# Kernel optimization log

Measured on AMD Instinct MI355X. Metric: run time of the kernel, lower is better.

## Reference

```python
import jax, jax.numpy as jnp
import numpy as np

ALPHA, GAMMA = 0.25, 2.0
IOU_THRES = 0.5
WEIGHTS = (10.0, 10.0, 5.0, 5.0, 15.0)
MAXV = 16  # max polygon verts during quad-vs-quad clipping (<=8, padded)


def box_corners(b):
    # b: (5,) = cx, cy, w, h, theta(rad); returns (4,2) CCW corners
    cx, cy, w, h, t = b[0], b[1], b[2], b[3], b[4]
    c, s = jnp.cos(t), jnp.sin(t)
    dx = jnp.array([-0.5, 0.5, 0.5, -0.5]) * w
    dy = jnp.array([-0.5, -0.5, 0.5, 0.5]) * h
    return jnp.stack([cx + dx * c - dy * s, cy + dx * s + dy * c], axis=-1)


def pair_iou(b1, b2):
    # exact rotated-rectangle IoU via Sutherland-Hodgman clipping
    p1 = box_corners(b1)
    p2 = box_corners(b2)
    poly = jnp.zeros((MAXV, 2)).at[:4].set(p1)
    n = jnp.int32(4)
    for e in range(4):
        a = p2[e]
        d = p2[(e + 1) % 4] - a
        out = jnp.zeros((MAXV, 2))
        m = jnp.int32(0)
        for i in range(MAXV):
            cur = poly[i]
            nxt = poly[jnp.where(i + 1 >= n, 0, i + 1)]
            sc = d[0] * (cur[1] - a[1]) - d[1] * (cur[0] - a[0])
            sn = d[0] * (nxt[1] - a[1]) - d[1] * (nxt[0] - a[0])
            valid = i < n
            keep = valid & (sc >= 0)
            out = out.at[m].set(jnp.where(keep, cur, out[m]))
            m = m + keep.astype(jnp.int32)
            crossed = valid & ((sc >= 0) != (sn >= 0))
            den = sc - sn
            t = sc / jnp.where(den == 0, 1.0, den)
            ip = cur + t * (nxt - cur)
            out = out.at[m].set(jnp.where(crossed, ip, out[m]))
            m = m + crossed.astype(jnp.int32)
        poly, n = out, m
    idx = jnp.arange(MAXV)
    nxt = jnp.where(idx + 1 >= n, 0, idx + 1)
    cr = poly[:, 0] * poly[nxt, 1] - poly[nxt, 0] * poly[:, 1]
    inter = 0.5 * jnp.abs(jnp.sum(jnp.where(idx < n, cr, 0.0)))
    union = b1[2] * b1[3] + b2[2] * b2[3] - inter
    return inter / jnp.maximum(union, 1e-9)


rbox_iou_mat = jax.vmap(jax.vmap(pair_iou, (None, 0)), (0, None))  # (A,5),(G,5)->(A,G)


def min_area_square(rb):
    s = jnp.maximum(rb[:, 2], rb[:, 3])
    return jnp.stack([rb[:, 0] - s / 2, rb[:, 1] - s / 2,
                      rb[:, 0] + s / 2, rb[:, 1] + s / 2], 1)


def bbox_overlaps(a, b):
    lt = jnp.maximum(a[:, None, :2], b[None, :, :2])
    rb = jnp.minimum(a[:, None, 2:], b[None, :, 2:])
    wh = jnp.clip(rb - lt, 0.0)
    inter = wh[..., 0] * wh[..., 1]
    aa = (a[:, 2] - a[:, 0]) * (a[:, 3] - a[:, 1])
    ab = (b[:, 2] - b[:, 0]) * (b[:, 3] - b[:, 1])
    return inter / jnp.maximum(aa[:, None] + ab[None, :] - inter, 1e-9)


def encode(ex, gt):
    wx, wy, ww, wh, wt = WEIGHTS
    ew = jnp.maximum(ex[:, 2], 1.0); eh = jnp.maximum(ex[:, 3], 1.0)
    gw = jnp.maximum(gt[:, 2], 1.0); gh = jnp.maximum(gt[:, 3], 1.0)
    dx = wx * (gt[:, 0] - ex[:, 0]) / ew
    dy = wy * (gt[:, 1] - ex[:, 1]) / eh
    dw = ww * jnp.log(gw / ew)
    dh = wh * jnp.log(gh / eh)
    dt = wt * (jnp.tan(gt[:, 4]) - jnp.tan(ex[:, 4]))
    return jnp.stack([dx, dy, dw, dh, dt], 1)


def lmr5pangle(anch, dt):
    # encoded angle offset of the 90-degree-swapped box: tan(t+pi/2) = -1/tan(t)
    wt = WEIGHTS[4]
    ta = jnp.tan(anch[:, 4])
    tg = dt / wt + ta
    tg = jnp.where(jnp.abs(tg) < 1e-4, jnp.where(tg < 0, -1e-4, 1e-4), tg)
    return wt * (-1.0 / tg - ta)


def landmark_encode(ex, lm):
    wx, wy = WEIGHTS[0], WEIGHTS[1]
    ew = jnp.maximum(ex[:, 2], 1.0); eh = jnp.maximum(ex[:, 3], 1.0)
    return jnp.stack([wx * (lm[:, 0] - ex[:, 0]) / ew,
                      wy * (lm[:, 1] - ex[:, 1]) / eh,
                      wx * (lm[:, 2] - ex[:, 0]) / ew,
                      wy * (lm[:, 3] - ex[:, 1]) / eh], 1)


def smooth_l1(d, beta=1.0 / 9):
    d = jnp.abs(d)
    return jnp.where(d < beta, 0.5 * d * d / beta, d - 0.5 * beta)


def lmr5p_per_anchor(pred, tgt, anch):
    t22 = lmr5pangle(anch, pred[:, 4])
    l1 = smooth_l1(tgt[:, 0] - pred[:, 0])
    l2 = smooth_l1(tgt[:, 1] - pred[:, 1])
    l3 = smooth_l1(tgt[:, 2] - pred[:, 2])
    l4 = smooth_l1(tgt[:, 3] - pred[:, 3])
    l5 = smooth_l1(tgt[:, 2] - pred[:, 3])  # |w1 - h2|
    l6 = smooth_l1(tgt[:, 3] - pred[:, 2])  # |h1 - w2|
    l7 = smooth_l1(tgt[:, 4] - pred[:, 4])
    l8 = smooth_l1(tgt[:, 4] - t22)
    return jnp.minimum(l1 + l2 + l3 + l4 + l7, l1 + l2 + l5 + l6 + l8)


def balanced_l1(d, beta=0.5, al=0.5, ga=0.9):
    d = jnp.abs(d)
    b = np.e ** (ga / al) - 1.0
    return jnp.where(d < beta,
                     al / b * (b * d + 1.0) * jnp.log(b * d / beta + 1.0) - al * d,
                     ga * d + ga / b - al * beta)


def per_image(cls, reg, lmk, anch, ann, ls):
    valid_g = ann[:, -1] != -1.0
    has_gt = jnp.any(valid_g)
    cls = jnp.clip(cls, 1e-4, 1.0 - 1e-4)
    indicator = bbox_overlaps(min_area_square(anch), min_area_square(ann[:, :5]))
    riou = rbox_iou_mat(anch, ann[:, :5])
    ious = jnp.where(indicator >= 0.1, riou, 0.0)   # rbox_overlaps thresh=0.1 gating
    ious = jnp.where(valid_g[None, :], ious, -1.0)  # mask padded gts
    ious = jax.lax.stop_gradient(ious)              # torch computes ious on cpu numpy
    iou_max = ious.max(1)
    iou_argmax = ious.argmax(1)
    pos = iou_max >= IOU_THRES
    max_gt = ious.max(0)
    argmax_gt = ious.argmax(0)
    force = valid_g & (max_gt < IOU_THRES)
    pos = (pos.astype(jnp.int32).at[argmax_gt].max(force.astype(jnp.int32))) > 0
    num_pos = pos.sum()
    denom = jnp.maximum(num_pos.astype(cls.dtype), 1.0)
    assigned = ann[iou_argmax]                       # (A, 6)
    lab = assigned[:, -1].astype(jnp.int32)
    onehot = (lab[:, None] == jnp.arange(cls.shape[-1])[None, :]).astype(cls.dtype)
    tgt = jnp.where(pos[:, None], onehot,
                    jnp.where((iou_max < IOU_THRES - 0.1)[:, None], 0.0, -1.0))
    af = jnp.where(tgt == 1.0, ALPHA, 1.0 - ALPHA)
    fw = af * jnp.where(tgt == 1.0, 1.0 - cls, cls) ** GAMMA
    bce = -(tgt * jnp.log(cls + 1e-6) + (1.0 - tgt) * jnp.log(1.0 - cls + 1e-6))
    cls_loss = jnp.where(tgt != -1.0, fw * bce, 0.0).sum() / denom
    cls_loss = jnp.where(has_gt, cls_loss, 0.0)
    gt_safe = jnp.where(pos[:, None], assigned[:, :5], anch)  # keep masked lanes finite
    tg1 = encode(anch, gt_safe)
    r1 = jnp.where(pos, lmr5p_per_anchor(reg, tg1, anch), 0.0).sum() / (5.0 * denom)
    r1 = jnp.where(has_gt & (num_pos > 0), r1, 0.0)
    lm_safe = jnp.where(pos[:, None], ls[iou_argmax],
                        jnp.stack([anch[:, 0], anch[:, 1], anch[:, 0], anch[:, 1]], 1))
    tg2 = landmark_encode(anch, lm_safe)
    r2 = jnp.where(pos[:, None], balanced_l1(lmk - tg2), 0.0).sum() / (4.0 * denom)
    r2 = jnp.where(has_gt & (num_pos > 0), r2, 0.0)
    return cls_loss, r1, r2


def setup_inputs() -> dict:
    B, A, G, C = 2, 16384, 24, 8
    NV = 16  # valid gts per image; remaining rows padded with label -1
    ks = jax.random.split(jax.random.key(0), 16)
    classifications = jax.random.uniform(ks[0], (B, A, C), jnp.float32)
    regressions = jax.random.normal(ks[1], (B, A, 5), jnp.float32) * 0.1
    landmarks = jax.random.normal(ks[2], (B, A, 4), jnp.float32) * 0.1
    gcx = 100.0 + 800.0 * jax.random.uniform(ks[3], (B, G))
    gcy = 100.0 + 800.0 * jax.random.uniform(ks[4], (B, G))
    gw = 40.0 + 160.0 * jax.random.uniform(ks[5], (B, G))
    gh = 40.0 + 160.0 * jax.random.uniform(ks[6], (B, G))
    gth = 1.2 * jax.random.uniform(ks[7], (B, G)) - 0.6
    lab = jax.random.randint(ks[8], (B, G), 0, C).astype(jnp.float32)
    lab = jnp.where(jnp.arange(G)[None, :] >= NV, -1.0, lab)
    annotations = jnp.stack([gcx, gcy, gw, gh, gth, lab], -1)
    acx = 1024.0 * jax.random.uniform(ks[9], (B, A))
    acy = 1024.0 * jax.random.uniform(ks[10], (B, A))
    aw = 16.0 + 112.0 * jax.random.uniform(ks[11], (B, A))
    ah = 16.0 + 112.0 * jax.random.uniform(ks[12], (B, A))
    ath = 1.2 * jax.random.uniform(ks[13], (B, A)) - 0.6
    anchors = jnp.stack([acx, acy, aw, ah, ath], -1)
    # plant jittered copies of the gts so a healthy number of anchors are positive
    jit = jax.random.normal(ks[14], (B, G, 5)) * jnp.array([2.0, 2.0, 2.0, 2.0, 0.01])
    anchors = anchors.at[:, :G, :].set(annotations[:, :, :5] + jit)
    ca, sa = jnp.cos(gth), jnp.sin(gth)
    gt_linestrips = jnp.stack([gcx - 0.4 * gw * ca, gcy - 0.4 * gw * sa,
                               gcx + 0.4 * gw * ca, gcy + 0.4 * gw * sa], -1)
    return {"classifications": classifications, "regressions": regressions,
            "anchors": anchors, "annotations": annotations,
            "landmarks": landmarks, "gt_linestrips": gt_linestrips}


def reference(classifications, regressions, anchors, annotations, landmarks, gt_linestrips):
    cls_l, r1, r2 = jax.vmap(per_image)(classifications, regressions, landmarks,
                                        anchors, annotations, gt_linestrips)
    return (cls_l.mean(keepdims=True), r1.mean(keepdims=True), r2.mean(keepdims=True))
```

## Files before the change

### kernel.cpp

```cpp
#include <hip/hip_runtime.h>
#include <math.h>

#define B_N 2
#define A_N 16384
#define G_N 24
#define C_N 8
#define NV  16
#define BPI 256

#define OFF_GTKEY  0
#define OFF_AKEY   384
#define OFF_PART   (384 + B_N * A_N * 8)

__device__ inline unsigned int fmap(float v) {
    unsigned int u = __float_as_uint(v);
    return (u & 0x80000000u) ? ~u : (u | 0x80000000u);
}
__device__ inline float funmap(unsigned int u) {
    unsigned int bits = (u & 0x80000000u) ? (u ^ 0x80000000u) : ~u;
    return __uint_as_float(bits);
}
__device__ inline unsigned long long mkkey(float v, int idx) {
    return ((unsigned long long)fmap(v) << 32) |
           (unsigned long long)(0xFFFFFFFFu - (unsigned int)idx);
}
__device__ inline float key_val(unsigned long long k) { return funmap((unsigned int)(k >> 32)); }
__device__ inline int   key_idx(unsigned long long k) { return (int)(0xFFFFFFFFu - (unsigned int)k); }

__device__ inline float smoothl1(float x) {
    const float beta = 1.0f / 9.0f;
    float d = fabsf(x);
    return (d < beta) ? (0.5f * d * d / beta) : (d - 0.5f * beta);
}
__device__ inline float balancedl1(float x) {
    const float bb  = 5.049647464412945f;
    const float alb = 0.5f / 5.049647464412945f;
    const float gab = 0.9f / 5.049647464412945f;
    float d = fabsf(x);
    if (d < 0.5f)
        return alb * (bb * d + 1.0f) * logf(bb * d / 0.5f + 1.0f) - 0.5f * d;
    return 0.9f * d + gab - 0.25f;
}
__device__ inline float focal_pos(const float* cr, int lab) {
    float s = 0.0f;
#pragma unroll
    for (int c = 0; c < C_N; c++) {
        float p = fminf(fmaxf(cr[c], 1e-4f), 0.9999f);
        if (c == lab) s += 0.25f * (1.0f - p) * (1.0f - p) * (-logf(p + 1e-6f));
        else          s += 0.75f * p * p * (-logf(1.0f - p + 1e-6f));
    }
    return s;
}
__device__ inline float focal_neg(const float* cr) {
    float s = 0.0f;
#pragma unroll
    for (int c = 0; c < C_N; c++) {
        float p = fminf(fmaxf(cr[c], 1e-4f), 0.9999f);
        s += 0.75f * p * p * (-logf(1.0f - p + 1e-6f));
    }
    return s;
}
__device__ inline float reg_loss(const float* rr, const float* ar, const float* annr) {
    float acx = ar[0], acy = ar[1], aw = ar[2], ah = ar[3], ath = ar[4];
    float aw1 = fmaxf(aw, 1.0f), ah1 = fmaxf(ah, 1.0f);
    float gw1 = fmaxf(annr[2], 1.0f), gh1 = fmaxf(annr[3], 1.0f);
    float t1 = 10.0f * (annr[0] - acx) / aw1;
    float t2 = 10.0f * (annr[1] - acy) / ah1;
    float t3 = 5.0f * logf(gw1 / aw1);
    float t4 = 5.0f * logf(gh1 / ah1);
    float ta = tanf(ath);
    float t5 = 15.0f * (tanf(annr[4]) - ta);
    float p0 = rr[0], p1 = rr[1], p2 = rr[2], p3 = rr[3], p4 = rr[4];
    float tg = p4 / 15.0f + ta;
    if (fabsf(tg) < 1e-4f) tg = (tg < 0.0f) ? -1e-4f : 1e-4f;
    float t22 = 15.0f * (-1.0f / tg - ta);
    float l1 = smoothl1(t1 - p0), l2 = smoothl1(t2 - p1);
    float l3 = smoothl1(t3 - p2), l4 = smoothl1(t4 - p3);
    float l5 = smoothl1(t3 - p3), l6 = smoothl1(t4 - p2);
    float l7 = smoothl1(t5 - p4), l8 = smoothl1(t5 - t22);
    return fminf(l1 + l2 + l3 + l4 + l7, l1 + l2 + l5 + l6 + l8);
}
__device__ inline float lmk_loss(const float* lk, const float* ar, const float* lr) {
    float acx = ar[0], acy = ar[1];
    float aw1 = fmaxf(ar[2], 1.0f), ah1 = fmaxf(ar[3], 1.0f);
    return balancedl1(lk[0] - 10.0f * (lr[0] - acx) / aw1)
         + balancedl1(lk[1] - 10.0f * (lr[1] - acy) / ah1)
         + balancedl1(lk[2] - 10.0f * (lr[2] - acx) / aw1)
         + balancedl1(lk[3] - 10.0f * (lr[3] - acy) / ah1);
}

__global__ __launch_bounds__(64) void k_main(
    const float* __restrict__ cls, const float* __restrict__ reg,
    const float* __restrict__ anch, const float* __restrict__ ann,
    const float* __restrict__ lmk, const float* __restrict__ ls,
    unsigned long long* __restrict__ gtkey, unsigned long long* __restrict__ akey,
    float* __restrict__ partials)
{
    __shared__ float pb[2][2][NV][64];
    __shared__ float gcor[G_N][10];
    __shared__ float gsq[G_N][5];
    __shared__ float glab[G_N];
    __shared__ float acor[9][64];
    __shared__ unsigned long long rowk[64];
    __shared__ unsigned short wl[G_N * 64];

    const int tid = threadIdx.x;
    const int b   = blockIdx.x >> 8;
    const int a   = ((blockIdx.x & (BPI - 1)) << 6) | tid;
    const size_t idx = (size_t)b * A_N + a;
    const float* annb = ann + (size_t)b * G_N * 6;

    const float* cr = cls + idx * C_N;
    float crv[C_N];
#pragma unroll
    for (int c = 0; c < C_N; c++) crv[c] = cr[c];

    const float* ar = anch + idx * 5;
    float acx = ar[0], acy = ar[1], aw = ar[2], ah = ar[3], ath = ar[4];

    if (tid < G_N) {
        const float* annr = annb + tid * 6;
        float gcx = annr[0], gcy = annr[1], gw = annr[2], gh = annr[3], gth = annr[4];
        glab[tid] = annr[5];
        float sg = fmaxf(gw, gh);
        float gx1 = gcx - sg * 0.5f, gy1 = gcy - sg * 0.5f;
        float gx2 = gcx + sg * 0.5f, gy2 = gcy + sg * 0.5f;
        gsq[tid][0] = gx1; gsq[tid][1] = gy1; gsq[tid][2] = gx2; gsq[tid][3] = gy2;
        gsq[tid][4] = (gx2 - gx1) * (gy2 - gy1);
        float c2 = cosf(gth), s2 = sinf(gth);
        const float dxs[4] = {-0.5f, 0.5f, 0.5f, -0.5f};
        const float dys[4] = {-0.5f, -0.5f, 0.5f, 0.5f};
#pragma unroll
        for (int k = 0; k < 4; k++) {
            float ex = dxs[k] * gw, ey = dys[k] * gh;
            gcor[tid][k]     = gcx + ex * c2 - ey * s2;
            gcor[tid][4 + k] = gcy + ex * s2 + ey * c2;
        }
        gcor[tid][8] = gw * gh;
    }
    if (a == 0) {
        for (int g = 0; g < G_N; g++)
            atomicMax(&gtkey[b * G_N + g], mkkey(0.0f, 0));
    }

    {
        float c1 = cosf(ath), s1 = sinf(ath);
        const float dxs[4] = {-0.5f, 0.5f, 0.5f, -0.5f};
        const float dys[4] = {-0.5f, -0.5f, 0.5f, 0.5f};
#pragma unroll
        for (int k = 0; k < 4; k++) {
            float dx = dxs[k] * aw, dy = dys[k] * ah;
            acor[k][tid]     = acx + dx * c1 - dy * s1;
            acor[4 + k][tid] = acy + dx * s1 + dy * c1;
        }
        acor[8][tid] = aw * ah;
    }
    __syncthreads();

    unsigned int validmask = 0;
    for (int g = 0; g < G_N; g++)
        if (glab[g] != -1.0f) validmask |= (1u << g);
    int first_valid = validmask ? (__ffs((int)validmask) - 1) : -1;

    rowk[tid] = (first_valid >= 0) ? mkkey(0.0f, first_valid) : 0ull;

    float sa = fmaxf(aw, ah);
    float ax1 = acx - sa * 0.5f, ay1 = acy - sa * 0.5f;
    float ax2 = acx + sa * 0.5f, ay2 = acy + sa * 0.5f;
    float areaA = (ax2 - ax1) * (ay2 - ay1);

    int cnt = 0;
    for (unsigned int vm = validmask; vm; vm &= vm - 1) {
        int g = __ffs((int)vm) - 1;
        float gx1 = gsq[g][0], gy1 = gsq[g][1], gx2 = gsq[g][2], gy2 = gsq[g][3];
        float iw = fmaxf(fminf(ax2, gx2) - fmaxf(ax1, gx1), 0.0f);
        float ih = fmaxf(fminf(ay2, gy2) - fmaxf(ay1, gy1), 0.0f);
        float inter0 = iw * ih;
        float ind = inter0 / fmaxf(areaA + gsq[g][4] - inter0, 1e-9f);
        bool pass = (ind >= 0.1f);
        unsigned long long bal = __ballot(pass);
        if (pass) {
            int off = __popcll(bal & ((1ull << tid) - 1ull));
            wl[cnt + off] = (unsigned short)((tid << 5) | g);
        }
        cnt += __popcll(bal);
    }
    __syncthreads();

    for (int i = tid; i < cnt; i += 64) {
        unsigned int e = wl[i];
        int owner = (int)(e >> 5);
        int g = (int)(e & 31u);
        float p2x[4], p2y[4];
#pragma unroll
        for (int k = 0; k < 4; k++) {
            p2x[k] = gcor[g][k];
            p2y[k] = gcor[g][4 + k];
            pb[0][0][k][tid] = acor[k][owner];
            pb[0][1][k][tid] = acor[4 + k][owner];
        }
        int n = 4, cb = 0;
#pragma unroll
        for (int e4 = 0; e4 < 4; e4++) {
            float apx = p2x[e4], apy = p2y[e4];
            float dx = p2x[(e4 + 1) & 3] - apx, dy = p2y[(e4 + 1) & 3] - apy;
            int m = 0, nb = cb ^ 1;
            for (int i2 = 0; i2 < n; i2++) {
                float cx_ = pb[cb][0][i2][tid], cy_ = pb[cb][1][i2][tid];
                int j = (i2 + 1 >= n) ? 0 : (i2 + 1);
                float nx_ = pb[cb][0][j][tid], ny_ = pb[cb][1][j][tid];
                float sc = dx * (cy_ - apy) - dy * (cx_ - apx);
                float sn = dx * (ny_ - apy) - dy * (nx_ - apx);
                bool ci = (sc >= 0.0f), niv = (sn >= 0.0f);
                if (ci) {
                    if (m < NV) { pb[nb][0][m][tid] = cx_; pb[nb][1][m][tid] = cy_; }
                    m++;
                }
                if (ci != niv) {
                    float den = sc - sn;
                    float t = sc / ((den == 0.0f) ? 1.0f : den);
                    if (m < NV) {
                        pb[nb][0][m][tid] = cx_ + t * (nx_ - cx_);
                        pb[nb][1][m][tid] = cy_ + t * (ny_ - cy_);
                    }
                    m++;
                }
            }
            n = (m > NV) ? NV : m;
            cb = nb;
        }
        float ssum = 0.0f;
        for (int i2 = 0; i2 < n; i2++) {
            int j = (i2 + 1 >= n) ? 0 : (i2 + 1);
            ssum += pb[cb][0][i2][tid] * pb[cb][1][j][tid]
                  - pb[cb][0][j][tid] * pb[cb][1][i2][tid];
        }
        float interA = 0.5f * fabsf(ssum);
        float uni = acor[8][owner] + gcor[g][8] - interA;
        float val = interA / fmaxf(uni, 1e-9f);

        atomicMax(&rowk[owner], mkkey(val, g));
        if (val > 0.0f) {
            int aowner = ((blockIdx.x & (BPI - 1)) << 6) | owner;
            atomicMax(&gtkey[b * G_N + g], mkkey(val, aowner));
        }
    }
    __syncthreads();

    unsigned long long rowkey = rowk[tid];
    akey[idx] = rowkey;

    float iou_max = key_val(rowkey);
    int gmax = key_idx(rowkey);
    const float* annr = annb + gmax * 6;
    float cls_sum = 0.0f, reg_sum = 0.0f, lmk_sum = 0.0f;
    int pc = 0;
    if (iou_max >= 0.5f) {
        pc = 1;
        cls_sum = focal_pos(crv, (int)annr[5]);
        reg_sum = reg_loss(reg + idx * 5, ar, annr);
        lmk_sum = lmk_loss(lmk + idx * 4, ar, ls + (size_t)(b * G_N + gmax) * 4);
    } else if (iou_max < 0.4f) {
        cls_sum = focal_neg(crv);
    }

    float fpc = (float)pc;
    for (int off = 32; off; off >>= 1) {
        cls_sum += __shfl_down(cls_sum, off);
        reg_sum += __shfl_down(reg_sum, off);
        lmk_sum += __shfl_down(lmk_sum, off);
        fpc     += __shfl_down(fpc, off);
    }
    if (tid == 0) {
        float* p = partials + (size_t)blockIdx.x * 4;
        p[0] = cls_sum; p[1] = reg_sum; p[2] = lmk_sum; p[3] = fpc;
    }
}

__global__ __launch_bounds__(128) void k_fix(
    const float* __restrict__ cls, const float* __restrict__ reg,
    const float* __restrict__ anch, const float* __restrict__ ann,
    const float* __restrict__ lmk, const float* __restrict__ ls,
    const unsigned long long* __restrict__ gtkey, const unsigned long long* __restrict__ akey,
    const float* __restrict__ partials, float* __restrict__ out)
{
    __shared__ float res[B_N][3];
    const int tid = threadIdx.x;
    const int b = tid >> 6, lane = tid & 63;

    double s0 = 0.0, s1 = 0.0, s2 = 0.0, s3 = 0.0;
    for (int r = lane; r < BPI; r += 64) {
        const float* p = partials + (size_t)(b * BPI + r) * 4;
        s0 += p[0]; s1 += p[1]; s2 += p[2]; s3 += p[3];
    }
    for (int off = 32; off; off >>= 1) {
        s0 += __shfl_down(s0, off);
        s1 += __shfl_down(s1, off);
        s2 += __shfl_down(s2, off);
        s3 += __shfl_down(s3, off);
    }

    const float* annb = ann + (size_t)b * G_N * 6;
    float dc = 0.0f, dr = 0.0f, dl = 0.0f; int dn = 0;
    if (lane < G_N) {
        bool valid = annb[lane * 6 + 5] != -1.0f;
        unsigned long long k = gtkey[b * G_N + lane];
        int fa = key_idx(k);
        bool force = valid && (key_val(k) < 0.5f);
        if (force) {
            for (int g2 = 0; g2 < lane; g2++) {
                if (annb[g2 * 6 + 5] == -1.0f) continue;
                unsigned long long k2 = gtkey[b * G_N + g2];
                if (key_val(k2) < 0.5f && key_idx(k2) == fa) { force = false; break; }
            }
        }
        if (force) {
            size_t fidx = (size_t)b * A_N + fa;
            unsigned long long ak = akey[fidx];
            float im = key_val(ak);
            if (!(im >= 0.5f)) {
                dn = 1;
                int gm = key_idx(ak);
                const float* cr = cls + fidx * C_N;
                float crv[C_N];
#pragma unroll
                for (int c = 0; c < C_N; c++) crv[c] = cr[c];
                const float* annr = annb + gm * 6;
                const float* arr = anch + fidx * 5;
                dc = focal_pos(crv, (int)annr[5]);
                if (im < 0.4f) dc -= focal_neg(crv);
                dr = reg_loss(reg + fidx * 5, arr, annr);
                dl = lmk_loss(lmk + fidx * 4, arr, ls + (size_t)(b * G_N + gm) * 4);
            }
        }
    }
    float fdn = (float)dn;
    for (int off = 32; off; off >>= 1) {
        dc  += __shfl_down(dc, off);
        dr  += __shfl_down(dr, off);
        dl  += __shfl_down(dl, off);
        fdn += __shfl_down(fdn, off);
    }
    if (lane == 0) {
        bool has_gt = false;
        for (int g = 0; g < G_N; g++)
            if (annb[g * 6 + 5] != -1.0f) has_gt = true;
        float np = (float)s3 + fdn;
        float denom = fmaxf(np, 1.0f);
        res[b][0] = has_gt ? (float)((s0 + dc) / denom) : 0.0f;
        res[b][1] = (has_gt && np > 0.0f) ? (float)((s1 + dr) / (5.0 * denom)) : 0.0f;
        res[b][2] = (has_gt && np > 0.0f) ? (float)((s2 + dl) / (4.0 * denom)) : 0.0f;
    }
    __syncthreads();
    if (tid == 0) {
        out[0] = (res[0][0] + res[1][0]) * 0.5f;
        out[1] = (res[0][1] + res[1][1]) * 0.5f;
        out[2] = (res[0][2] + res[1][2]) * 0.5f;
    }
}

extern "C" void kernel_launch(void* const* d_in, const int* in_sizes, int n_in,
                              void* d_out, int out_size, void* d_ws, size_t ws_size,
                              hipStream_t stream)
{
    (void)in_sizes; (void)n_in; (void)out_size; (void)ws_size;
    const float* cls  = (const float*)d_in[0];
    const float* reg  = (const float*)d_in[1];
    const float* anch = (const float*)d_in[2];
    const float* ann  = (const float*)d_in[3];
    const float* lmk  = (const float*)d_in[4];
    const float* ls   = (const float*)d_in[5];

    char* ws = (char*)d_ws;
    unsigned long long* gtkey = (unsigned long long*)(ws + OFF_GTKEY);
    unsigned long long* akey  = (unsigned long long*)(ws + OFF_AKEY);
    float* partials = (float*)(ws + OFF_PART);
    float* out = (float*)d_out;

    hipMemsetAsync(gtkey, 0, B_N * G_N * 8, stream);
    hipLaunchKernelGGL(k_main, dim3(B_N * BPI), dim3(64), 0, stream,
                       cls, reg, anch, ann, lmk, ls, gtkey, akey, partials);
    hipLaunchKernelGGL(k_fix, dim3(1), dim3(128), 0, stream,
                       cls, reg, anch, ann, lmk, ls, gtkey, akey, partials, out);
}
```

Measured before the change: 103.9 us.

## Precompute GT table in a prep kernel and restructure polygon clipping

Adds a small prep kernel that builds a per-GT record table (corners, square box, tan, landmarks, label) plus a valid mask, replacing the memset and the per-block GT setup and atomics. The main kernel copies the table into LDS with float4 loads and vectorises the class-score loads. The clipping is restructured: the first edge clips from registers, the middle edges use float2 LDS buffers capped at 8 vertices, and the last edge accumulates the shoelace area directly without storing. This trades an extra kernel launch for less per-block setup and fewer LDS round trips, and it relies on the clipped polygon never exceeding 8 vertices.

```diff
diff --git a/kernel.cpp b/kernel.cpp
--- a/kernel.cpp
+++ b/kernel.cpp
@@ -5,12 +5,16 @@
 #define A_N 16384
 #define G_N 24
 #define C_N 8
-#define NV  16
+#define NV8 8
 #define BPI 256
+#define RECF 32
+#define RECL 33
 
 #define OFF_GTKEY  0
-#define OFF_AKEY   384
-#define OFF_PART   (384 + B_N * A_N * 8)
+#define OFF_META   384
+#define OFF_GTAB   512
+#define OFF_AKEY   (512 + 6144)
+#define OFF_PART   (OFF_AKEY + B_N * A_N * 8)
 
 __device__ inline unsigned int fmap(float v) {
     unsigned int u = __float_as_uint(v);
@@ -59,6 +63,34 @@
         s += 0.75f * p * p * (-logf(1.0f - p + 1e-6f));
     }
     return s;
+}
+__device__ inline float reg_loss_v(const float* rr, float acx, float acy, float aw,
+                                   float ah, float ath, const float* gl) {
+    float aw1 = fmaxf(aw, 1.0f), ah1 = fmaxf(ah, 1.0f);
+    float gw1 = fmaxf(gl[16], 1.0f), gh1 = fmaxf(gl[17], 1.0f);
+    float t1 = 10.0f * (gl[14] - acx) / aw1;
+    float t2 = 10.0f * (gl[15] - acy) / ah1;
+    float t3 = 5.0f * logf(gw1 / aw1);
+    float t4 = 5.0f * logf(gh1 / ah1);
+    float ta = tanf(ath);
+    float t5 = 15.0f * (gl[20] - ta);
+    float p0 = rr[0], p1 = rr[1], p2 = rr[2], p3 = rr[3], p4 = rr[4];
+    float tg = p4 / 15.0f + ta;
+    if (fabsf(tg) < 1e-4f) tg = (tg < 0.0f) ? -1e-4f : 1e-4f;
+    float t22 = 15.0f * (-1.0f / tg - ta);
+    float l1 = smoothl1(t1 - p0), l2 = smoothl1(t2 - p1);
+    float l3 = smoothl1(t3 - p2), l4 = smoothl1(t4 - p3);
+    float l5 = smoothl1(t3 - p3), l6 = smoothl1(t4 - p2);
+    float l7 = smoothl1(t5 - p4), l8 = smoothl1(t5 - t22);
+    return fminf(l1 + l2 + l3 + l4 + l7, l1 + l2 + l5 + l6 + l8);
+}
+__device__ inline float lmk_loss_v(const float* lk, float acx, float acy, float aw,
+                                   float ah, const float* gl) {
+    float aw1 = fmaxf(aw, 1.0f), ah1 = fmaxf(ah, 1.0f);
+    return balancedl1(lk[0] - 10.0f * (gl[21] - acx) / aw1)
+         + balancedl1(lk[1] - 10.0f * (gl[22] - acy) / ah1)
+         + balancedl1(lk[2] - 10.0f * (gl[23] - acx) / aw1)
+         + balancedl1(lk[3] - 10.0f * (gl[24] - acy) / ah1);
 }
 __device__ inline float reg_loss(const float* rr, const float* ar, const float* annr) {
     float acx = ar[0], acy = ar[1], aw = ar[2], ah = ar[3], ath = ar[4];
@@ -89,18 +121,61 @@
          + balancedl1(lk[3] - 10.0f * (lr[3] - acy) / ah1);
 }
 
+__global__ __launch_bounds__(64) void k_pre(
+    const float* __restrict__ ann, const float* __restrict__ ls,
+    float* __restrict__ gtab, unsigned long long* __restrict__ gtkey,
+    int2* __restrict__ meta)
+{
+    int t = threadIdx.x;
+    if (t < B_N * G_N) {
+        const float* annr = ann + (size_t)t * 6;
+        float gcx = annr[0], gcy = annr[1], gw = annr[2], gh = annr[3];
+        float gth = annr[4], lab = annr[5];
+        float* r = gtab + (size_t)t * RECF;
+        float c2 = cosf(gth), s2 = sinf(gth);
+        const float dxs[4] = {-0.5f, 0.5f, 0.5f, -0.5f};
+        const float dys[4] = {-0.5f, -0.5f, 0.5f, 0.5f};
+#pragma unroll
+        for (int k = 0; k < 4; k++) {
+            float ex = dxs[k] * gw, ey = dys[k] * gh;
+            r[k]     = gcx + ex * c2 - ey * s2;
+            r[4 + k] = gcy + ex * s2 + ey * c2;
+        }
+        r[8] = gw * gh;
+        float sg = fmaxf(gw, gh);
+        float gx1 = gcx - sg * 0.5f, gy1 = gcy - sg * 0.5f;
+        float gx2 = gcx + sg * 0.5f, gy2 = gcy + sg * 0.5f;
+        r[9] = gx1; r[10] = gy1; r[11] = gx2; r[12] = gy2;
+        r[13] = (gx2 - gx1) * (gy2 - gy1);
+        r[14] = gcx; r[15] = gcy; r[16] = gw; r[17] = gh; r[18] = gth; r[19] = lab;
+        r[20] = tanf(gth);
+        const float* lr = ls + (size_t)t * 4;
+        r[21] = lr[0]; r[22] = lr[1]; r[23] = lr[2]; r[24] = lr[3];
+#pragma unroll
+        for (int k = 25; k < RECF; k++) r[k] = 0.0f;
+        gtkey[t] = (lab != -1.0f) ? mkkey(0.0f, 0) : 0ull;
+    }
+    if (t < B_N * G_N && (t % G_N) == 0) {
+        int b = t / G_N;
+        unsigned int vm = 0; int fv = -1;
+        for (int g = 0; g < G_N; g++) {
+            float lab = ann[(size_t)(t + g) * 6 + 5];
+            if (lab != -1.0f) { vm |= (1u << g); if (fv < 0) fv = g; }
+        }
+        meta[b] = make_int2((int)vm, fv);
+    }
+}
+
 __global__ __launch_bounds__(64) void k_main(
     const float* __restrict__ cls, const float* __restrict__ reg,
-    const float* __restrict__ anch, const float* __restrict__ ann,
-    const float* __restrict__ lmk, const float* __restrict__ ls,
+    const float* __restrict__ anch, const float* __restrict__ lmk,
+    const float* __restrict__ gtab, const int2* __restrict__ meta,
     unsigned long long* __restrict__ gtkey, unsigned long long* __restrict__ akey,
     float* __restrict__ partials)
 {
-    __shared__ float pb[2][2][NV][64];
-    __shared__ float gcor[G_N][10];
-    __shared__ float gsq[G_N][5];
-    __shared__ float glab[G_N];
-    __shared__ float acor[9][64];
+    __shared__ float  glds[G_N * RECL];
+    __shared__ float2 pb2[2 * NV8 * 64];
+    __shared__ float  acor[9][64];
     __shared__ unsigned long long rowk[64];
     __shared__ unsigned short wl[G_N * 64];
 
@@ -108,61 +183,42 @@
     const int b   = blockIdx.x >> 8;
     const int a   = ((blockIdx.x & (BPI - 1)) << 6) | tid;
     const size_t idx = (size_t)b * A_N + a;
-    const float* annb = ann + (size_t)b * G_N * 6;
-
-    const float* cr = cls + idx * C_N;
-    float crv[C_N];
-#pragma unroll
-    for (int c = 0; c < C_N; c++) crv[c] = cr[c];
-
+
+    const int2 mv = meta[b];
     const float* ar = anch + idx * 5;
     float acx = ar[0], acy = ar[1], aw = ar[2], ah = ar[3], ath = ar[4];
-
-    if (tid < G_N) {
-        const float* annr = annb + tid * 6;
-        float gcx = annr[0], gcy = annr[1], gw = annr[2], gh = annr[3], gth = annr[4];
-        glab[tid] = annr[5];
-        float sg = fmaxf(gw, gh);
-        float gx1 = gcx - sg * 0.5f, gy1 = gcy - sg * 0.5f;
-        float gx2 = gcx + sg * 0.5f, gy2 = gcy + sg * 0.5f;
-        gsq[tid][0] = gx1; gsq[tid][1] = gy1; gsq[tid][2] = gx2; gsq[tid][3] = gy2;
-        gsq[tid][4] = (gx2 - gx1) * (gy2 - gy1);
-        float c2 = cosf(gth), s2 = sinf(gth);
+    float4 c0 = ((const float4*)cls)[idx * 2];
+    float4 c1 = ((const float4*)cls)[idx * 2 + 1];
+    float crv[C_N] = {c0.x, c0.y, c0.z, c0.w, c1.x, c1.y, c1.z, c1.w};
+
+    {
+        const float4* gt4 = (const float4*)gtab + (size_t)b * G_N * (RECF / 4);
+        for (int t = tid; t < G_N * (RECF / 4); t += 64) {
+            float4 v = gt4[t];
+            int rec = t >> 3, q = t & 7;
+            float* d = glds + rec * RECL + q * 4;
+            d[0] = v.x; d[1] = v.y; d[2] = v.z; d[3] = v.w;
+        }
+    }
+    float axk[4], ayk[4];
+    {
+        float c1_ = cosf(ath), s1_ = sinf(ath);
         const float dxs[4] = {-0.5f, 0.5f, 0.5f, -0.5f};
         const float dys[4] = {-0.5f, -0.5f, 0.5f, 0.5f};
 #pragma unroll
         for (int k = 0; k < 4; k++) {
-            float ex = dxs[k] * gw, ey = dys[k] * gh;
-            gcor[tid][k]     = gcx + ex * c2 - ey * s2;
-            gcor[tid][4 + k] = gcy + ex * s2 + ey * c2;
-        }
-        gcor[tid][8] = gw * gh;
-    }
-    if (a == 0) {
-        for (int g = 0; g < G_N; g++)
-            atomicMax(&gtkey[b * G_N + g], mkkey(0.0f, 0));
-    }
-
-    {
-        float c1 = cosf(ath), s1 = sinf(ath);
-        const float dxs[4] = {-0.5f, 0.5f, 0.5f, -0.5f};
-        const float dys[4] = {-0.5f, -0.5f, 0.5f, 0.5f};
-#pragma unroll
-        for (int k = 0; k < 4; k++) {
             float dx = dxs[k] * aw, dy = dys[k] * ah;
-            acor[k][tid]     = acx + dx * c1 - dy * s1;
-            acor[4 + k][tid] = acy + dx * s1 + dy * c1;
+            axk[k] = acx + dx * c1_ - dy * s1_;
+            ayk[k] = acy + dx * s1_ + dy * c1_;
+            acor[k][tid] = axk[k];
+            acor[4 + k][tid] = ayk[k];
         }
         acor[8][tid] = aw * ah;
     }
+    unsigned int validmask = (unsigned int)mv.x;
+    int first_valid = mv.y;
+    rowk[tid] = (first_valid >= 0) ? mkkey(0.0f, first_valid) : 0ull;
     __syncthreads();
-
-    unsigned int validmask = 0;
-    for (int g = 0; g < G_N; g++)
-        if (glab[g] != -1.0f) validmask |= (1u << g);
-    int first_valid = validmask ? (__ffs((int)validmask) - 1) : -1;
-
-    rowk[tid] = (first_valid >= 0) ? mkkey(0.0f, first_valid) : 0ull;
 
     float sa = fmaxf(aw, ah);
     float ax1 = acx - sa * 0.5f, ay1 = acy - sa * 0.5f;
@@ -172,11 +228,11 @@
     int cnt = 0;
     for (unsigned int vm = validmask; vm; vm &= vm - 1) {
         int g = __ffs((int)vm) - 1;
-        float gx1 = gsq[g][0], gy1 = gsq[g][1], gx2 = gsq[g][2], gy2 = gsq[g][3];
-        float iw = fmaxf(fminf(ax2, gx2) - fmaxf(ax1, gx1), 0.0f);
-        float ih = fmaxf(fminf(ay2, gy2) - fmaxf(ay1, gy1), 0.0f);
+        const float* gq = glds + g * RECL;
+        float iw = fmaxf(fminf(ax2, gq[11]) - fmaxf(ax1, gq[9]), 0.0f);
+        float ih = fmaxf(fminf(ay2, gq[12]) - fmaxf(ay1, gq[10]), 0.0f);
         float inter0 = iw * ih;
-        float ind = inter0 / fmaxf(areaA + gsq[g][4] - inter0, 1e-9f);
+        float ind = inter0 / fmaxf(areaA + gq[13] - inter0, 1e-9f);
         bool pass = (ind >= 0.1f);
         unsigned long long bal = __ballot(pass);
         if (pass) {
@@ -191,52 +247,109 @@
         unsigned int e = wl[i];
         int owner = (int)(e >> 5);
         int g = (int)(e & 31u);
+        const float* gl = glds + g * RECL;
         float p2x[4], p2y[4];
 #pragma unroll
-        for (int k = 0; k < 4; k++) {
-            p2x[k] = gcor[g][k];
-            p2y[k] = gcor[g][4 + k];
-            pb[0][0][k][tid] = acor[k][owner];
-            pb[0][1][k][tid] = acor[4 + k][owner];
-        }
-        int n = 4, cb = 0;
-#pragma unroll
-        for (int e4 = 0; e4 < 4; e4++) {
-            float apx = p2x[e4], apy = p2y[e4];
-            float dx = p2x[(e4 + 1) & 3] - apx, dy = p2y[(e4 + 1) & 3] - apy;
-            int m = 0, nb = cb ^ 1;
-            for (int i2 = 0; i2 < n; i2++) {
-                float cx_ = pb[cb][0][i2][tid], cy_ = pb[cb][1][i2][tid];
-                int j = (i2 + 1 >= n) ? 0 : (i2 + 1);
-                float nx_ = pb[cb][0][j][tid], ny_ = pb[cb][1][j][tid];
-                float sc = dx * (cy_ - apy) - dy * (cx_ - apx);
-                float sn = dx * (ny_ - apy) - dy * (nx_ - apx);
+        for (int k = 0; k < 4; k++) { p2x[k] = gl[k]; p2y[k] = gl[4 + k]; }
+        float ax_[4], ay_[4];
+#pragma unroll
+        for (int k = 0; k < 4; k++) { ax_[k] = acor[k][owner]; ay_[k] = acor[4 + k][owner]; }
+
+        int n;
+        {
+            float apx = p2x[0], apy = p2y[0];
+            float dxe = p2x[1] - apx, dye = p2y[1] - apy;
+            int m = 0;
+#pragma unroll
+            for (int v = 0; v < 4; v++) {
+                float cx_ = ax_[v], cy_ = ay_[v];
+                float nx_ = ax_[(v + 1) & 3], ny_ = ay_[(v + 1) & 3];
+                float sc = dxe * (cy_ - apy) - dye * (cx_ - apx);
+                float sn = dxe * (ny_ - apy) - dye * (nx_ - apx);
                 bool ci = (sc >= 0.0f), niv = (sn >= 0.0f);
                 if (ci) {
-                    if (m < NV) { pb[nb][0][m][tid] = cx_; pb[nb][1][m][tid] = cy_; }
+                    if (m < NV8) pb2[(0 * NV8 + m) * 64 + tid] = make_float2(cx_, cy_);
                     m++;
                 }
                 if (ci != niv) {
                     float den = sc - sn;
                     float t = sc / ((den == 0.0f) ? 1.0f : den);
-                    if (m < NV) {
-                        pb[nb][0][m][tid] = cx_ + t * (nx_ - cx_);
-                        pb[nb][1][m][tid] = cy_ + t * (ny_ - cy_);
-                    }
+                    if (m < NV8) pb2[(0 * NV8 + m) * 64 + tid] =
+                        make_float2(cx_ + t * (nx_ - cx_), cy_ + t * (ny_ - cy_));
                     m++;
                 }
             }
-            n = (m > NV) ? NV : m;
-            cb = nb;
+            n = m;
+        }
+        for (int eidx = 1; eidx <= 2; eidx++) {
+            int src = (eidx == 1) ? 0 : 1;
+            int dst = (eidx == 1) ? 1 : 0;
+            float apx = p2x[eidx], apy = p2y[eidx];
+            float dxe = p2x[(eidx + 1) & 3] - apx, dye = p2y[(eidx + 1) & 3] - apy;
+            int m = 0;
+            if (n > 0) {
+                float2 first = pb2[(src * NV8 + 0) * 64 + tid];
+                float2 cur = first;
+                float2 pref = (n > 1) ? pb2[(src * NV8 + 1) * 64 + tid] : first;
+                for (int v = 0; v < n; v++) {
+                    float2 nxt = (v + 1 < n) ? pref : first;
+                    if (v + 2 < n) pref = pb2[(src * NV8 + v + 2) * 64 + tid];
+                    float sc = dxe * (cur.y - apy) - dye * (cur.x - apx);
+                    float sn = dxe * (nxt.y - apy) - dye * (nxt.x - apx);
+                    bool ci = (sc >= 0.0f), niv = (sn >= 0.0f);
+                    if (ci) {
+                        if (m < NV8) pb2[(dst * NV8 + m) * 64 + tid] = cur;
+                        m++;
+                    }
+                    if (ci != niv) {
+                        float den = sc - sn;
+                        float t = sc / ((den == 0.0f) ? 1.0f : den);
+                        if (m < NV8) pb2[(dst * NV8 + m) * 64 + tid] =
+                            make_float2(cur.x + t * (nxt.x - cur.x), cur.y + t * (nxt.y - cur.y));
+                        m++;
+                    }
+                    cur = nxt;
+                }
+            }
+            n = m;
         }
         float ssum = 0.0f;
-        for (int i2 = 0; i2 < n; i2++) {
-            int j = (i2 + 1 >= n) ? 0 : (i2 + 1);
-            ssum += pb[cb][0][i2][tid] * pb[cb][1][j][tid]
-                  - pb[cb][0][j][tid] * pb[cb][1][i2][tid];
+        {
+            float apx = p2x[3], apy = p2y[3];
+            float dxe = p2x[0] - apx, dye = p2y[0] - apy;
+            float2 efirst = make_float2(0.0f, 0.0f), eprev = efirst;
+            int fcnt = 0;
+            if (n > 0) {
+                float2 first = pb2[(0 * NV8 + 0) * 64 + tid];
+                float2 cur = first;
+                float2 pref = (n > 1) ? pb2[(0 * NV8 + 1) * 64 + tid] : first;
+                for (int v = 0; v < n; v++) {
+                    float2 nxt = (v + 1 < n) ? pref : first;
+                    if (v + 2 < n) pref = pb2[(0 * NV8 + v + 2) * 64 + tid];
+                    float sc = dxe * (cur.y - apy) - dye * (cur.x - apx);
+                    float sn = dxe * (nxt.y - apy) - dye * (nxt.x - apx);
+                    bool ci = (sc >= 0.0f), niv = (sn >= 0.0f);
+                    if (ci) {
+                        if (fcnt == 0) efirst = cur;
+                        else ssum += eprev.x * cur.y - cur.x * eprev.y;
+                        eprev = cur; fcnt++;
+                    }
+                    if (ci != niv) {
+                        float den = sc - sn;
+                        float t = sc / ((den == 0.0f) ? 1.0f : den);
+                        float2 ip = make_float2(cur.x + t * (nxt.x - cur.x),
+                                                cur.y + t * (nxt.y - cur.y));
+                        if (fcnt == 0) efirst = ip;
+                        else ssum += eprev.x * ip.y - ip.x * eprev.y;
+                        eprev = ip; fcnt++;
+                    }
+                    cur = nxt;
+                }
+            }
+            if (fcnt > 0) ssum += eprev.x * efirst.y - efirst.x * eprev.y;
         }
         float interA = 0.5f * fabsf(ssum);
-        float uni = acor[8][owner] + gcor[g][8] - interA;
+        float uni = acor[8][owner] + gl[8] - interA;
         float val = interA / fmaxf(uni, 1e-9f);
 
         atomicMax(&rowk[owner], mkkey(val, g));
@@ -252,14 +365,14 @@
 
     float iou_max = key_val(rowkey);
     int gmax = key_idx(rowkey);
-    const float* annr = annb + gmax * 6;
     float cls_sum = 0.0f, reg_sum = 0.0f, lmk_sum = 0.0f;
     int pc = 0;
     if (iou_max >= 0.5f) {
+        const float* gl = glds + gmax * RECL;
         pc = 1;
-        cls_sum = focal_pos(crv, (int)annr[5]);
-        reg_sum = reg_loss(reg + idx * 5, ar, annr);
-        lmk_sum = lmk_loss(lmk + idx * 4, ar, ls + (size_t)(b * G_N + gmax) * 4);
+        cls_sum = focal_pos(crv, (int)gl[19]);
+        reg_sum = reg_loss_v(reg + idx * 5, acx, acy, aw, ah, ath, gl);
+        lmk_sum = lmk_loss_v(lmk + idx * 4, acx, acy, aw, ah, gl);
     } else if (iou_max < 0.4f) {
         cls_sum = focal_neg(crv);
     }
@@ -373,13 +486,15 @@
 
     char* ws = (char*)d_ws;
     unsigned long long* gtkey = (unsigned long long*)(ws + OFF_GTKEY);
-    unsigned long long* akey  = (unsigned long long*)(ws + OFF_AKEY);
+    int2*  meta  = (int2*)(ws + OFF_META);
+    float* gtab  = (float*)(ws + OFF_GTAB);
+    unsigned long long* akey = (unsigned long long*)(ws + OFF_AKEY);
     float* partials = (float*)(ws + OFF_PART);
     float* out = (float*)d_out;
 
-    hipMemsetAsync(gtkey, 0, B_N * G_N * 8, stream);
+    hipLaunchKernelGGL(k_pre, dim3(1), dim3(64), 0, stream, ann, ls, gtab, gtkey, meta);
     hipLaunchKernelGGL(k_main, dim3(B_N * BPI), dim3(64), 0, stream,
-                       cls, reg, anch, ann, lmk, ls, gtkey, akey, partials);
+                       cls, reg, anch, lmk, gtab, meta, gtkey, akey, partials);
     hipLaunchKernelGGL(k_fix, dim3(1), dim3(128), 0, stream,
                        cls, reg, anch, ann, lmk, ls, gtkey, akey, partials, out);
 }
```

Result: no change. 104.6 us (+0.7%).
